# Performance work log

Hardware: AMD Instinct MI355X
Metric: run time of the kernel (lower is better)

Reference implementation:

```python
import jax, jax.numpy as jnp
import numpy as np

CHUNK = 64
L2_EPS = 1e-6
RMS_EPS = 1e-5


def _silu(x):
    return x * jax.nn.sigmoid(x)


def _causal_shared_conv(x, w):
    # x: [B,T,C]; w: [K] single kernel shared across all channels (depthwise).
    K = w.shape[0]
    T = x.shape[1]
    xp = jnp.pad(x, ((0, 0), (K - 1, 0), (0, 0)))
    out = w[0] * xp[:, 0:T, :]
    for j in range(1, K):  # K=4, tiny fixed loop
        out = out + w[j] * xp[:, j:j + T, :]
    return out


def _l2norm(x):
    return x * jax.lax.rsqrt(jnp.sum(x * x, axis=-1, keepdims=True) + L2_EPS)


def _delta_rule_chunk(q, k, v, beta, chunk=CHUNK):
    # q,k: [B,H,T,dk]; v: [B,H,T,dv]; beta: [B,H,T]
    B, H, T, dk = q.shape
    dv = v.shape[-1]
    q = q * (dk ** -0.5)
    nC = T // chunk
    q = q.reshape(B, H, nC, chunk, dk)
    k = k.reshape(B, H, nC, chunk, dk)
    v = v.reshape(B, H, nC, chunk, dv)
    beta = beta.reshape(B, H, nC, chunk)
    k_beta = k * beta[..., None]
    v_beta = v * beta[..., None]
    # UT transform: invert the unit-lower-triangular (I + stril(K_beta K^T))
    A = jnp.einsum('bhncd,bhnmd->bhncm', k_beta, k)  # [B,H,nC,C,C]
    stril = jnp.tril(jnp.ones((chunk, chunk), bool), -1)
    M = jnp.where(stril, A, 0.0) + jnp.eye(chunk, dtype=q.dtype)
    u = jax.scipy.linalg.solve_triangular(M, v_beta, lower=True)  # T @ (beta*v)
    w = jax.scipy.linalg.solve_triangular(M, k_beta, lower=True)  # T @ (beta*k)
    tril_incl = jnp.tril(jnp.ones((chunk, chunk), bool))

    def step(S, inp):
        q_i, k_i, u_i, w_i = inp  # [B,H,C,d*]
        u_i = u_i - jnp.einsum('bhcd,bhde->bhce', w_i, S)
        attn = jnp.where(tril_incl, jnp.einsum('bhcd,bhmd->bhcm', q_i, k_i), 0.0)
        o_i = jnp.einsum('bhcd,bhde->bhce', q_i, S) + jnp.einsum('bhcm,bhme->bhce', attn, u_i)
        S = S + jnp.einsum('bhcd,bhce->bhde', k_i, u_i)
        return S, o_i

    xs = tuple(jnp.moveaxis(t, 2, 0) for t in (q, k, u, w))
    S0 = jnp.zeros((B, H, dk, dv), q.dtype)
    _, o = jax.lax.scan(step, S0, xs)  # o: [nC,B,H,C,dv]
    return jnp.moveaxis(o, 0, 2).reshape(B, H, T, dv)


def setup_inputs() -> dict:
    key = jax.random.key(0)
    ks = jax.random.split(key, 10)
    B, T, D, H = 2, 4096, 2048, 16
    sc = 0.02
    return {
        'x': jax.random.normal(ks[0], (B, T, D), jnp.float32),
        'Wq': jax.random.normal(ks[1], (D, D), jnp.float32) * sc,
        'Wk': jax.random.normal(ks[2], (D, D), jnp.float32) * sc,
        'Wv': jax.random.normal(ks[3], (D, D), jnp.float32) * sc,
        'Wb': jax.random.normal(ks[4], (D, H), jnp.float32) * sc,
        'Wo': jax.random.normal(ks[5], (D, D), jnp.float32) * sc,
        'conv_q': jax.random.normal(ks[6], (4,), jnp.float32) * 0.5,
        'conv_k': jax.random.normal(ks[7], (4,), jnp.float32) * 0.5,
        'conv_v': jax.random.normal(ks[8], (4,), jnp.float32) * 0.5,
        'onorm_w': jnp.ones((D // H,), jnp.float32),
    }


def reference(x, Wq, Wk, Wv, Wb, Wo, conv_q, conv_k, conv_v, onorm_w):
    B, T, D = x.shape
    H = Wb.shape[1]
    dk = Wq.shape[1] // H
    dv = Wv.shape[1] // H
    # projections + shared-kernel causal short conv (silu activation)
    q = _silu(_causal_shared_conv(x @ Wq, conv_q))
    k = _silu(_causal_shared_conv(x @ Wk, conv_k))
    v = _silu(_causal_shared_conv(x @ Wv, conv_v))
    beta = jax.nn.sigmoid(x @ Wb)  # [B,T,H]
    # split heads -> [B,H,T,d]
    qh = _l2norm(q.reshape(B, T, H, dk)).transpose(0, 2, 1, 3)
    kh = _l2norm(k.reshape(B, T, H, dk)).transpose(0, 2, 1, 3)
    vh = v.reshape(B, T, H, dv).transpose(0, 2, 1, 3)
    o = _delta_rule_chunk(qh, kh, vh, beta.transpose(0, 2, 1))  # [B,H,T,dv]
    o = o.transpose(0, 2, 1, 3)  # [B,T,H,dv]
    # per-head RMSNorm over head_v_dim
    o = o * jax.lax.rsqrt(jnp.mean(o * o, axis=-1, keepdims=True) + RMS_EPS) * onorm_w
    return o.reshape(B, T, H * dv) @ Wo
```

## Files before the change

### kernel.cpp

```cpp
#include <hip/hip_runtime.h>
#include <math.h>

#define B_ 2
#define T_ 4096
#define D_ 2048
#define H_ 16
#define DK 128
#define DV 128
#define CH 64
#define M_ (B_ * T_)
#define NCH (T_ / CH)

typedef __attribute__((ext_vector_type(8))) short bfrag;
typedef __attribute__((ext_vector_type(4))) float ffrag;
typedef __attribute__((ext_vector_type(8))) unsigned short u16x8;
typedef unsigned short us;

#define MFMA __builtin_amdgcn_mfma_f32_16x16x32_bf16

__device__ inline us f2bf(float f) {
  union { float f; unsigned u; } v; v.f = f;
  unsigned r = v.u + 0x7fffu + ((v.u >> 16) & 1u);
  return (us)(r >> 16);
}
__device__ inline float bf2f(us u) {
  union { unsigned u; float f; } v; v.u = ((unsigned)u) << 16;
  return v.f;
}

__device__ inline void gl_lds16(const us* g, us* l) {
  __builtin_amdgcn_global_load_lds(
      (const __attribute__((address_space(1))) void*)g,
      (__attribute__((address_space(3))) void*)l, 16, 0, 0);
}

__global__ __launch_bounds__(256) void to_bf16(const float* __restrict__ in,
                                               us* __restrict__ out) {
  const size_t i = ((size_t)blockIdx.x * 256 + threadIdx.x) * 8;
  const float4 a = *reinterpret_cast<const float4*>(in + i);
  const float4 b = *reinterpret_cast<const float4*>(in + i + 4);
  ushort4 o0, o1;
  o0.x = f2bf(a.x); o0.y = f2bf(a.y); o0.z = f2bf(a.z); o0.w = f2bf(a.w);
  o1.x = f2bf(b.x); o1.y = f2bf(b.y); o1.z = f2bf(b.z); o1.w = f2bf(b.w);
  *reinterpret_cast<ushort4*>(out + i) = o0;
  *reinterpret_cast<ushort4*>(out + i + 4) = o1;
}

__global__ __launch_bounds__(256) void wtrans(const float* __restrict__ W,
                                              us* __restrict__ Wt) {
  __shared__ float tile[64][68];
  const int k0 = blockIdx.y * 64, n0 = blockIdx.x * 64;
  const int lr = threadIdx.x >> 4, lc = (threadIdx.x & 15) * 4;
#pragma unroll
  for (int p = 0; p < 4; ++p) {
    const int r = lr + p * 16;
    *reinterpret_cast<float4*>(&tile[r][lc]) =
        *reinterpret_cast<const float4*>(&W[(size_t)(k0 + r) * D_ + n0 + lc]);
  }
  __syncthreads();
#pragma unroll
  for (int p = 0; p < 4; ++p) {
    const int r = lr + p * 16;
    ushort4 o;
    o.x = f2bf(tile[lc + 0][r]); o.y = f2bf(tile[lc + 1][r]);
    o.z = f2bf(tile[lc + 2][r]); o.w = f2bf(tile[lc + 3][r]);
    *reinterpret_cast<ushort4*>(&Wt[(size_t)(n0 + r) * D_ + k0 + lc]) = o;
  }
}

template <bool OUTF32>
__global__ __launch_bounds__(512, 2) void gemm256(const us* __restrict__ A,
                                                  const us* __restrict__ Bt,
                                                  void* __restrict__ Cp,
                                                  int M, int N, int K) {
  __shared__ __align__(16) us lds[2][2][2][256 * 32];
  const int t = threadIdx.x, l = t & 63, w = t >> 6;
  const int wm = w >> 2, wn = w & 3;
  const int fr = l & 15, hi = l >> 4;
  const int sx = 8 * (hi ^ ((fr >> 1) & 3));

  const int m0 = blockIdx.y * 256;
  const int n0 = blockIdx.x * 256;

  const int srow = t >> 2;
  const int scol = 8 * ((t & 3) ^ ((t >> 3) & 3));
  const us* Ab = A + (size_t)(m0 + srow) * K + scol;
  const us* Bb = Bt + (size_t)(n0 + srow) * K + scol;

  ffrag acc[8][4];
#pragma unroll
  for (int mi = 0; mi < 8; ++mi)
#pragma unroll
    for (int ni = 0; ni < 4; ++ni)
#pragma unroll
      for (int e = 0; e < 4; ++e) acc[mi][ni][e] = 0.f;

#define STG_A(bf, kk, kt)                                                      \
  do {                                                                         \
    gl_lds16(Ab + (size_t)(kt) * 64 + (kk) * 32, &lds[bf][0][kk][t * 8]);      \
    gl_lds16(Ab + (size_t)128 * K + (size_t)(kt) * 64 + (kk) * 32,             \
             &lds[bf][0][kk][4096 + t * 8]);                                   \
  } while (0)
#define STG_B(bf, kk, kt)                                                      \
  do {                                                                         \
    gl_lds16(Bb + (size_t)(kt) * 64 + (kk) * 32, &lds[bf][1][kk][t * 8]);      \
    gl_lds16(Bb + (size_t)128 * K + (size_t)(kt) * 64 + (kk) * 32,             \
             &lds[bf][1][kk][4096 + t * 8]);                                   \
  } while (0)

  const int NT = K >> 6;
  STG_A(0, 0, 0); STG_B(0, 0, 0); STG_A(0, 1, 0); STG_B(0, 1, 0);
  asm volatile("s_waitcnt vmcnt(4)" ::: "memory");
  __builtin_amdgcn_s_barrier();
  __builtin_amdgcn_sched_barrier(0);

  const int arow = wm * 128 + fr;
  const int brow = wn * 64 + fr;

#pragma unroll 1
  for (int kt = 0; kt < NT; ++kt) {
    const int cur = kt & 1, oth = cur ^ 1;
    const bool pf = (kt + 1 < NT);
    bfrag af4[4], bf4[4];

    {
      const us* pa = &lds[cur][0][0][0];
      const us* pb = &lds[cur][1][0][0];
#pragma unroll
      for (int ni = 0; ni < 4; ++ni)
        bf4[ni] = *reinterpret_cast<const bfrag*>(pb + (brow + ni * 16) * 32 + sx);
#pragma unroll
      for (int mi = 0; mi < 4; ++mi)
        af4[mi] = *reinterpret_cast<const bfrag*>(pa + (arow + mi * 16) * 32 + sx);
      if (pf) STG_A(oth, 0, kt + 1);
      __builtin_amdgcn_s_setprio(1);
#pragma unroll
      for (int mi = 0; mi < 4; ++mi)
#pragma unroll
        for (int ni = 0; ni < 4; ++ni)
          acc[mi][ni] = MFMA(af4[mi], bf4[ni], acc[mi][ni], 0, 0, 0);
      __builtin_amdgcn_s_setprio(0);
#pragma unroll
      for (int mi = 0; mi < 4; ++mi)
        af4[mi] = *reinterpret_cast<const bfrag*>(pa + (arow + 64 + mi * 16) * 32 + sx);
      if (pf) STG_B(oth, 0, kt + 1);
      __builtin_amdgcn_s_setprio(1);
#pragma unroll
      for (int mi = 0; mi < 4; ++mi)
#pragma unroll
        for (int ni = 0; ni < 4; ++ni)
          acc[mi + 4][ni] = MFMA(af4[mi], bf4[ni], acc[mi + 4][ni], 0, 0, 0);
      __builtin_amdgcn_s_setprio(0);
    }
    if (pf) asm volatile("s_waitcnt vmcnt(4)" ::: "memory");
    else    asm volatile("s_waitcnt vmcnt(0)" ::: "memory");
    __builtin_amdgcn_s_barrier();
    __builtin_amdgcn_sched_barrier(0);

    {
      const us* pa = &lds[cur][0][1][0];
      const us* pb = &lds[cur][1][1][0];
#pragma unroll
      for (int ni = 0; ni < 4; ++ni)
        bf4[ni] = *reinterpret_cast<const bfrag*>(pb + (brow + ni * 16) * 32 + sx);
#pragma unroll
      for (int mi = 0; mi < 4; ++mi)
        af4[mi] = *reinterpret_cast<const bfrag*>(pa + (arow + mi * 16) * 32 + sx);
      if (pf) STG_A(oth, 1, kt + 1);
      __builtin_amdgcn_s_setprio(1);
#pragma unroll
      for (int mi = 0; mi < 4; ++mi)
#pragma unroll
        for (int ni = 0; ni < 4; ++ni)
          acc[mi][ni] = MFMA(af4[mi], bf4[ni], acc[mi][ni], 0, 0, 0);
      __builtin_amdgcn_s_setprio(0);
#pragma unroll
      for (int mi = 0; mi < 4; ++mi)
        af4[mi] = *reinterpret_cast<const bfrag*>(pa + (arow + 64 + mi * 16) * 32 + sx);
      if (pf) STG_B(oth, 1, kt + 1);
      __builtin_amdgcn_s_setprio(1);
#pragma unroll
      for (int mi = 0; mi < 4; ++mi)
#pragma unroll
        for (int ni = 0; ni < 4; ++ni)
          acc[mi + 4][ni] = MFMA(af4[mi], bf4[ni], acc[mi + 4][ni], 0, 0, 0);
      __builtin_amdgcn_s_setprio(0);
    }
    if (pf) asm volatile("s_waitcnt vmcnt(4)" ::: "memory");
    else    asm volatile("s_waitcnt vmcnt(0)" ::: "memory");
    __builtin_amdgcn_s_barrier();
    __builtin_amdgcn_sched_barrier(0);
  }
#undef STG_A
#undef STG_B

  const int crow = m0 + wm * 128 + hi * 4;
  const int ccol = n0 + wn * 64 + fr;
#pragma unroll
  for (int mi = 0; mi < 8; ++mi)
#pragma unroll
    for (int ni = 0; ni < 4; ++ni)
#pragma unroll
      for (int j = 0; j < 4; ++j) {
        const size_t idx = (size_t)(crow + mi * 16 + j) * N + ccol + ni * 16;
        if constexpr (OUTF32) ((float*)Cp)[idx] = acc[mi][ni][j];
        else ((us*)Cp)[idx] = f2bf(acc[mi][ni][j]);
      }
}

__device__ inline void conv_body(const us* __restrict__ in, const float* cw,
                                 int bt, int d0, int mode, float v[8]) {
  const int tb = bt & (T_ - 1);
  const us* row = in + (size_t)bt * D_ + d0;
#pragma unroll
  for (int j = 0; j < 8; ++j) v[j] = 0.f;
#pragma unroll
  for (int j = 0; j < 4; ++j) {
    if (tb >= j) {
      const us* rp = row - (size_t)(j * D_);
      const ushort4 a = *reinterpret_cast<const ushort4*>(rp);
      const ushort4 b = *reinterpret_cast<const ushort4*>(rp + 4);
      const float wj = cw[3 - j];
      v[0] = fmaf(wj, bf2f(a.x), v[0]); v[1] = fmaf(wj, bf2f(a.y), v[1]);
      v[2] = fmaf(wj, bf2f(a.z), v[2]); v[3] = fmaf(wj, bf2f(a.w), v[3]);
      v[4] = fmaf(wj, bf2f(b.x), v[4]); v[5] = fmaf(wj, bf2f(b.y), v[5]);
      v[6] = fmaf(wj, bf2f(b.z), v[6]); v[7] = fmaf(wj, bf2f(b.w), v[7]);
    }
  }
#pragma unroll
  for (int j = 0; j < 8; ++j) v[j] = v[j] / (1.f + expf(-v[j]));
  if (mode) {
    float ss = 0.f;
#pragma unroll
    for (int j = 0; j < 8; ++j) ss = fmaf(v[j], v[j], ss);
    ss += __shfl_xor(ss, 1);
    ss += __shfl_xor(ss, 2);
    ss += __shfl_xor(ss, 4);
    ss += __shfl_xor(ss, 8);
    float sc = rsqrtf(ss + 1e-6f);
    if (mode == 2) sc *= 0.08838834764831845f;
#pragma unroll
    for (int j = 0; j < 8; ++j) v[j] *= sc;
  }
}

__global__ __launch_bounds__(256) void conv_silu_plain(const us* __restrict__ in,
                                                       const float* __restrict__ cw,
                                                       us* __restrict__ out) {
  const int bt = blockIdx.x, d0 = threadIdx.x * 8;
  float v[8];
  conv_body(in, cw, bt, d0, 0, v);
  ushort4 o0, o1;
  o0.x = f2bf(v[0]); o0.y = f2bf(v[1]); o0.z = f2bf(v[2]); o0.w = f2bf(v[3]);
  o1.x = f2bf(v[4]); o1.y = f2bf(v[5]); o1.z = f2bf(v[6]); o1.w = f2bf(v[7]);
  us* op = out + (size_t)bt * D_ + d0;
  *reinterpret_cast<ushort4*>(op) = o0;
  *reinterpret_cast<ushort4*>(op + 4) = o1;
}

__global__ __launch_bounds__(256) void conv_silu_chunk(const us* __restrict__ in,
                                                       const float* __restrict__ cw,
                                                       us* __restrict__ out,
                                                       int mode) {
  const int bt = blockIdx.x, d0 = threadIdx.x * 8;
  float v[8];
  conv_body(in, cw, bt, d0, mode, v);
  const int b = bt >> 12, tt = bt & (T_ - 1);
  const int cid = tt >> 6, r = tt & 63;
  const int h = d0 >> 7, g = (d0 & 127) >> 3;
  us* dst = out + ((size_t)((b * H_ + h) * NCH + cid)) * (CH * DK) +
            r * 128 + ((g ^ (r & 15)) * 8);
  ushort4 o0, o1;
  o0.x = f2bf(v[0]); o0.y = f2bf(v[1]); o0.z = f2bf(v[2]); o0.w = f2bf(v[3]);
  o1.x = f2bf(v[4]); o1.y = f2bf(v[5]); o1.z = f2bf(v[6]); o1.w = f2bf(v[7]);
  *reinterpret_cast<ushort4*>(dst) = o0;
  *reinterpret_cast<ushort4*>(dst + 4) = o1;
}

__global__ __launch_bounds__(256) void beta_sigmoid(const float* __restrict__ x,
                                                    const float* __restrict__ Wb,
                                                    float* __restrict__ betaT) {
  const int t = threadIdx.x;
  const int m = blockIdx.x * 4 + (t >> 6);
  const int l = t & 63;
  const int c = l & 15;
  const int s = l >> 4;
  const float* xr = x + (size_t)m * D_;
  const int kb = s * (D_ / 4);
  float acc = 0.f;
  for (int k = 0; k < D_ / 4; ++k)
    acc = fmaf(xr[kb + k], Wb[(size_t)(kb + k) * H_ + c], acc);
  acc += __shfl_xor(acc, 16);
  acc += __shfl_xor(acc, 32);
  if (l < 16) {
    const int b = m >> 12, tt = m & (T_ - 1);
    betaT[((size_t)(b * H_ + c)) * T_ + tt] = 1.f / (1.f + expf(-acc));
  }
}

__device__ inline void prod_step(float* Tf, const float* Am, float* xbuf,
                                 int r, int c, int I, int J,
                                 int nk, int K0, int K1, int K2) {
  float X = 0.f;
  const int Ks[3] = {K0, K1, K2};
  for (int kk = 0; kk < nk; ++kk) {
    const int K = Ks[kk];
    const float* amrow = Am + (16 * I + r) * 72 + 16 * K;
    const float* tcol = Tf + (16 * K) * 68 + 16 * J + c;
#pragma unroll
    for (int m = 0; m < 16; ++m) X = fmaf(amrow[m], tcol[m * 68], X);
  }
  __syncthreads();
  xbuf[r * 17 + c] = X;
  __syncthreads();
  float s = 0.f;
  const float* trow = Tf + (16 * I + r) * 68 + 16 * I;
#pragma unroll
  for (int m = 0; m < 16; ++m) s = fmaf(trow[m], xbuf[m * 17 + c], s);
  Tf[(16 * I + r) * 68 + 16 * J + c] = -s;
  __syncthreads();
}

__global__ __launch_bounds__(256, 2) void delta_prep(const us* __restrict__ qch,
                                                     const us* __restrict__ kch,
                                                     const float* __restrict__ betaT,
                                                     us* __restrict__ v_uv,
                                                     us* __restrict__ Wout,
                                                     us* __restrict__ kTout,
                                                     us* __restrict__ Aout) {
  __shared__ __align__(16) unsigned char lds[72000];
  us*    ks    = (us*)(lds);
  us*    Tb    = (us*)(lds);
  float* Am    = (float*)(lds + 16384);
  us*    vTb   = (us*)(lds + 16384);
  float* Tf    = (float*)(lds + 34816);
  us*    atst  = (us*)(lds + 34816);
  us*    Wst   = (us*)(lds + 34816);
  us*    kTb   = (us*)(lds + 52224);
  us*    UVst  = (us*)(lds + 52224);
  float* betac = (float*)(lds + 70656);
  float* xbuf  = (float*)(lds + 70912);

  const int t = threadIdx.x, w = t >> 6, l = t & 63;
  const int rr = l & 15, hi = l >> 4;
  const int bx = blockIdx.x;
  const int bh = bx >> 6, cid = bx & 63;
  const int b = bh >> 4, h = bh & 15;
  const size_t rowbase = ((size_t)b * T_ + (size_t)cid * CH) * D_ + (size_t)h * DK;
  const size_t cbase = (size_t)bx * (CH * DK);
  const size_t abase = (size_t)bx * (CH * CH);

  {
    const us* kg = kch + cbase;
#pragma unroll
    for (int p = 0; p < 4; ++p)
      gl_lds16(kg + p * 2048 + t * 8, ks + p * 2048 + t * 8);
    const float4 z = make_float4(0.f, 0.f, 0.f, 0.f);
    *reinterpret_cast<float4*>(atst + t * 16) = z;
    *reinterpret_cast<float4*>(atst + t * 16 + 8) = z;
    if (t < 64) betac[t] = betaT[(size_t)bh * T_ + cid * CH + t];
  }
  __syncthreads();

  {
    bfrag qf[4], kf[4];
#pragma unroll
    for (int k4 = 0; k4 < 4; ++k4) {
      const int go = ((4 * k4 + hi) ^ rr) * 8;
      qf[k4] = *reinterpret_cast<const bfrag*>(qch + cbase + (16 * w + rr) * 128 + go);
      kf[k4] = *reinterpret_cast<const bfrag*>(ks + (16 * w + rr) * 128 + go);
    }
    for (int jt = 0; jt <= w; ++jt) {
      ffrag accA = {0.f, 0.f, 0.f, 0.f}, accQ = {0.f, 0.f, 0.f, 0.f};
#pragma unroll
      for (int k4 = 0; k4 < 4; ++k4) {
        const bfrag bfr = *reinterpret_cast<const bfrag*>(
            ks + (16 * jt + rr) * 128 + (((4 * k4 + hi) ^ rr) * 8));
        accA = MFMA(kf[k4], bfr, accA, 0, 0, 0);
        accQ = MFMA(qf[k4], bfr, accQ, 0, 0, 0);
      }
// ... 61 lines not shown
    const int vr = t >> 2, vp = t & 3;
    u16x8 vv[4];
#pragma unroll
    for (int g = 0; g < 4; ++g)
      vv[g] = *reinterpret_cast<const u16x8*>(v_uv + rowbase + (size_t)vr * D_ +
                                              vp * 32 + g * 8);
    const int ti = t >> 2, tg = t & 3;
    u16x8 w0, w1;
#pragma unroll
    for (int jj = 0; jj < 8; ++jj) {
      const int j0 = tg * 16 + jj, j1 = j0 + 8;
      w0[jj] = f2bf(Tf[ti * 68 + j0] * betac[j0]);
      w1[jj] = f2bf(Tf[ti * 68 + j1] * betac[j1]);
    }
    *reinterpret_cast<u16x8*>(Tb + ti * 72 + tg * 16) = w0;
    *reinterpret_cast<u16x8*>(Tb + ti * 72 + tg * 16 + 8) = w1;
#pragma unroll
    for (int g = 0; g < 4; ++g)
#pragma unroll
      for (int j = 0; j < 8; ++j)
        vTb[(vp * 32 + g * 8 + j) * 72 + vr] = vv[g][j];
  }
  __syncthreads();

  {
    bfrag ta[2];
#pragma unroll
    for (int k2 = 0; k2 < 2; ++k2)
      ta[k2] = *reinterpret_cast<const bfrag*>(Tb + (16 * w + rr) * 72 + 32 * k2 + 8 * hi);
#pragma unroll
    for (int dt = 0; dt < 8; ++dt) {
      ffrag acc = {0.f, 0.f, 0.f, 0.f};
#pragma unroll
      for (int k2 = 0; k2 < 2; ++k2) {
        const bfrag bfr = *reinterpret_cast<const bfrag*>(
            kTb + (16 * dt + rr) * 72 + 32 * k2 + 8 * hi);
        acc = MFMA(ta[k2], bfr, acc, 0, 0, 0);
      }
#pragma unroll
      for (int j4 = 0; j4 < 4; ++j4) {
        const int i = 16 * w + 4 * hi + j4, d = 16 * dt + rr;
        Wst[i * 128 + (((d >> 3) ^ (i & 15)) * 8) + (d & 7)] = f2bf(-acc[j4]);
      }
    }
  }
  __syncthreads();

  {
    bfrag ta[2];
#pragma unroll
    for (int k2 = 0; k2 < 2; ++k2)
      ta[k2] = *reinterpret_cast<const bfrag*>(Tb + (16 * w + rr) * 72 + 32 * k2 + 8 * hi);
#pragma unroll
    for (int et = 0; et < 8; ++et) {
      ffrag acc = {0.f, 0.f, 0.f, 0.f};
#pragma unroll
      for (int k2 = 0; k2 < 2; ++k2) {
        const bfrag bfr = *reinterpret_cast<const bfrag*>(
            vTb + (16 * et + rr) * 72 + 32 * k2 + 8 * hi);
        acc = MFMA(ta[k2], bfr, acc, 0, 0, 0);
      }
#pragma unroll
      for (int j4 = 0; j4 < 4; ++j4)
        UVst[(16 * w + 4 * hi + j4) * 128 + 16 * et + rr] = f2bf(acc[j4]);
    }
#pragma unroll
    for (int p = 0; p < 4; ++p) {
      const int unit = t + p * 256;
      *reinterpret_cast<u16x8*>(Wout + cbase + unit * 8) =
          *reinterpret_cast<const u16x8*>(Wst + unit * 8);
    }
  }
  __syncthreads();

#pragma unroll
  for (int p = 0; p < 4; ++p) {
    const int unit = t + p * 256;
    const int r = unit >> 4, g = unit & 15;
    *reinterpret_cast<u16x8*>(v_uv + rowbase + (size_t)r * D_ + g * 8) =
        *reinterpret_cast<const u16x8*>(UVst + r * 128 + g * 8);
  }
}

__global__ __launch_bounds__(256, 1) void delta_seq(const us* __restrict__ qch,
                                                    const us* __restrict__ Wch,
                                                    const us* __restrict__ kTch,
                                                    const us* __restrict__ atch,
                                                    us* __restrict__ uv_o) {
  __shared__ __align__(16) us qs[2][CH * DK];
  __shared__ __align__(16) us Ws[2][CH * DK];
  __shared__ __align__(16) us kTs[2][DK * CH];
  __shared__ __align__(16) us ats[2][CH * CH];
  __shared__ __align__(16) us uvs[2][CH * 16];
  __shared__ __align__(16) us Sb[2][16 * 136];
  __shared__ __align__(16) us ub[CH * 18];

  const int t = threadIdx.x, l = t & 63, w = t >> 6;
  const int bx = blockIdx.x;
  const int vs = bx >> 5, bh = bx & 31;
  const int b = bh >> 4, h = bh & 15;
  const int rr = l & 15, hi = l >> 4;

  ffrag sacc[2];
#pragma unroll
  for (int t2 = 0; t2 < 2; ++t2)
#pragma unroll
    for (int j = 0; j < 4; ++j) sacc[t2][j] = 0.f;

  for (int i = t; i < 16 * 136; i += 256) Sb[0][i] = 0;

  const size_t cbQ = (size_t)(bh * NCH) * (CH * DK);
  const size_t cbA = (size_t)(bh * NCH) * (CH * CH);
  const size_t rowbase0 = ((size_t)b * T_) * D_ + (size_t)h * DK + vs * 16;

#define STAGE(buf, cid)                                                        \
  do {                                                                         \
    const us* qg = qch + cbQ + (size_t)(cid) * (CH * DK);                      \
    const us* Wg = Wch + cbQ + (size_t)(cid) * (CH * DK);                      \
    const us* kg = kTch + cbQ + (size_t)(cid) * (CH * DK);                     \
    const us* ag = atch + cbA + (size_t)(cid) * (CH * CH);                     \
    _Pragma("unroll")                                                          \
    for (int p = 0; p < 4; ++p) {                                              \
      gl_lds16(qg + p * 2048 + t * 8, &qs[buf][p * 2048 + t * 8]);             \
      gl_lds16(Wg + p * 2048 + t * 8, &Ws[buf][p * 2048 + t * 8]);             \
      gl_lds16(kg + p * 2048 + t * 8, &kTs[buf][p * 2048 + t * 8]);            \
    }                                                                          \
    _Pragma("unroll")                                                          \
    for (int p = 0; p < 2; ++p)                                                \
      gl_lds16(ag + p * 2048 + t * 8, &ats[buf][p * 2048 + t * 8]);            \
    if (t < 128)                                                               \
      gl_lds16(uv_o + rowbase0 + (size_t)((cid) * CH + (t >> 1)) * D_ + (t & 1) * 8, \
               &uvs[buf][t * 8]);                                              \
  } while (0)

  STAGE(0, 0);
  asm volatile("s_waitcnt vmcnt(0) lgkmcnt(0)" ::: "memory");
  __builtin_amdgcn_s_barrier();
  __builtin_amdgcn_sched_barrier(0);

  for (int cid = 0; cid < NCH; ++cid) {
    const int cur = cid & 1;
    if (cid + 1 < NCH) STAGE(cur ^ 1, cid + 1);

    bfrag sbf[4];
#pragma unroll
    for (int ks = 0; ks < 4; ++ks)
      sbf[ks] = *reinterpret_cast<const bfrag*>(&Sb[cur][rr * 136 + ks * 32 + hi * 8]);

    {
      ffrag uacc;
#pragma unroll
      for (int j = 0; j < 4; ++j)
        uacc[j] = bf2f(uvs[cur][(16 * w + 4 * hi + j) * 16 + rr]);
#pragma unroll
      for (int ks = 0; ks < 4; ++ks) {
        const bfrag af = *reinterpret_cast<const bfrag*>(
            &Ws[cur][(16 * w + rr) * 128 + (((4 * ks + hi) ^ rr) * 8)]);
        uacc = MFMA(af, sbf[ks], uacc, 0, 0, 0);
      }
#pragma unroll
      for (int j = 0; j < 4; ++j)
        ub[(16 * w + 4 * hi + j) * 18 + rr] = f2bf(uacc[j]);
    }
    asm volatile("s_waitcnt lgkmcnt(0)" ::: "memory");
    __builtin_amdgcn_s_barrier();
    __builtin_amdgcn_sched_barrier(0);

    {
      ffrag oacc;
#pragma unroll
      for (int j = 0; j < 4; ++j) oacc[j] = 0.f;
#pragma unroll
      for (int ks = 0; ks < 4; ++ks) {
        const bfrag af = *reinterpret_cast<const bfrag*>(
            &qs[cur][(16 * w + rr) * 128 + (((4 * ks + hi) ^ rr) * 8)]);
        oacc = MFMA(af, sbf[ks], oacc, 0, 0, 0);
      }
      const int nks = (w < 2) ? 1 : 2;
      for (int ks = 0; ks < nks; ++ks) {
        bfrag ubf;
#pragma unroll
        for (int j = 0; j < 8; ++j)
          ubf[j] = (short)ub[(32 * ks + 8 * hi + j) * 18 + rr];
        const bfrag af = *reinterpret_cast<const bfrag*>(
            &ats[cur][(16 * w + rr) * 64 + (((4 * ks + hi) ^ (rr & 7)) * 8)]);
        oacc = MFMA(af, ubf, oacc, 0, 0, 0);
      }
      us* og = uv_o + rowbase0 + (size_t)(cid * CH) * D_;
#pragma unroll
      for (int j = 0; j < 4; ++j)
        og[(size_t)(16 * w + 4 * hi + j) * D_ + rr] = f2bf(oacc[j]);
    }

    {
      bfrag ubf[2];
#pragma unroll
      for (int ks = 0; ks < 2; ++ks)
#pragma unroll
        for (int j = 0; j < 8; ++j)
          ubf[ks][j] = (short)ub[(32 * ks + 8 * hi + j) * 18 + rr];
#pragma unroll
      for (int t2 = 0; t2 < 2; ++t2) {
        const int tile = 2 * w + t2;
#pragma unroll
        for (int ks = 0; ks < 2; ++ks) {
          const bfrag af = *reinterpret_cast<const bfrag*>(
              &kTs[cur][(16 * tile + rr) * 64 + (((4 * ks + hi) ^ (rr & 7)) * 8)]);
          sacc[t2] = MFMA(af, ubf[ks], sacc[t2], 0, 0, 0);
        }
        ushort4 sw;
        sw.x = f2bf(sacc[t2][0]); sw.y = f2bf(sacc[t2][1]);
        sw.z = f2bf(sacc[t2][2]); sw.w = f2bf(sacc[t2][3]);
        *reinterpret_cast<ushort4*>(&Sb[cur ^ 1][rr * 136 + 16 * tile + 4 * hi]) = sw;
      }
    }
    asm volatile("s_waitcnt vmcnt(0) lgkmcnt(0)" ::: "memory");
    __builtin_amdgcn_s_barrier();
    __builtin_amdgcn_sched_barrier(0);
  }
#undef STAGE
}

__global__ __launch_bounds__(256) void rms_onorm_bf16(const us* __restrict__ in,
                                                      const float* __restrict__ w,
                                                      us* __restrict__ out) {
  const int bt = blockIdx.x;
  const int d0 = threadIdx.x * 8;
  const us* p = in + (size_t)bt * D_ + d0;
  const ushort4 a = *reinterpret_cast<const ushort4*>(p);
  const ushort4 b = *reinterpret_cast<const ushort4*>(p + 4);
  float v[8] = {bf2f(a.x), bf2f(a.y), bf2f(a.z), bf2f(a.w),
                bf2f(b.x), bf2f(b.y), bf2f(b.z), bf2f(b.w)};
  float ss = 0.f;
#pragma unroll
  for (int j = 0; j < 8; ++j) ss = fmaf(v[j], v[j], ss);
  ss += __shfl_xor(ss, 1);
  ss += __shfl_xor(ss, 2);
  ss += __shfl_xor(ss, 4);
  ss += __shfl_xor(ss, 8);
  const float sc = rsqrtf(ss * (1.0f / 128.0f) + 1e-5f);
  const int hd = d0 & 127;
  ushort4 o0, o1;
  o0.x = f2bf(v[0] * sc * w[hd + 0]); o0.y = f2bf(v[1] * sc * w[hd + 1]);
  o0.z = f2bf(v[2] * sc * w[hd + 2]); o0.w = f2bf(v[3] * sc * w[hd + 3]);
  o1.x = f2bf(v[4] * sc * w[hd + 4]); o1.y = f2bf(v[5] * sc * w[hd + 5]);
  o1.z = f2bf(v[6] * sc * w[hd + 6]); o1.w = f2bf(v[7] * sc * w[hd + 7]);
  us* op = out + (size_t)bt * D_ + d0;
  *reinterpret_cast<ushort4*>(op) = o0;
  *reinterpret_cast<ushort4*>(op + 4) = o1;
}

extern "C" void kernel_launch(void* const* d_in, const int* in_sizes, int n_in,
                              void* d_out, int out_size, void* d_ws, size_t ws_size,
                              hipStream_t stream) {
  const float* x  = (const float*)d_in[0];
  const float* Wq = (const float*)d_in[1];
  const float* Wk = (const float*)d_in[2];
  const float* Wv = (const float*)d_in[3];
  const float* Wb = (const float*)d_in[4];
  const float* Wo = (const float*)d_in[5];
  const float* cq = (const float*)d_in[6];
  const float* ck = (const float*)d_in[7];
  const float* cv = (const float*)d_in[8];
  const float* ow = (const float*)d_in[9];
  float* out = (float*)d_out;

  const size_t NE = (size_t)M_ * D_;
  us* ws   = (us*)d_ws;
  us* gout = ws;
  us* qch  = ws + NE;
  us* kch  = ws + 2 * NE;
  us* Wch  = ws + 3 * NE;
  us* kTch = ws + 4 * NE;
  us* wt   = ws + 5 * NE;
  us* attb = gout;
  float* betaT = (float*)(gout + 12 * 1024 * 1024);
  us* xb = (us*)d_out;
  us* vb = xb + NE;

  dim3 gg(D_ / 256, M_ / 256);
  dim3 wg(D_ / 64, D_ / 64);

  to_bf16<<<NE / 2048, 256, 0, stream>>>(x, xb);

  wtrans<<<wg, 256, 0, stream>>>(Wv, wt);
  gemm256<false><<<gg, 512, 0, stream>>>(xb, wt, gout, M_, D_, D_);
  conv_silu_plain<<<M_, 256, 0, stream>>>(gout, cv, vb);

  wtrans<<<wg, 256, 0, stream>>>(Wq, wt);
  gemm256<false><<<gg, 512, 0, stream>>>(xb, wt, gout, M_, D_, D_);
  conv_silu_chunk<<<M_, 256, 0, stream>>>(gout, cq, qch, 2);

  wtrans<<<wg, 256, 0, stream>>>(Wk, wt);
  gemm256<false><<<gg, 512, 0, stream>>>(xb, wt, gout, M_, D_, D_);
  conv_silu_chunk<<<M_, 256, 0, stream>>>(gout, ck, kch, 1);

  beta_sigmoid<<<M_ / 4, 256, 0, stream>>>(x, Wb, betaT);

  delta_prep<<<32 * NCH, 256, 0, stream>>>(qch, kch, betaT, vb, Wch, kTch, attb);
  delta_seq<<<256, 256, 0, stream>>>(qch, Wch, kTch, attb, vb);

  rms_onorm_bf16<<<M_, 256, 0, stream>>>(vb, ow, kTch);

  wtrans<<<wg, 256, 0, stream>>>(Wo, wt);
  gemm256<true><<<gg, 512, 0, stream>>>(kTch, wt, out, M_, D_, D_);
}
```

Baseline: 650.9 us.

## Split delta_seq into 512-thread specialized warps for state update and output

The sequential delta-rule kernel now launches 512 threads. Warps 0-3 compute u and the state update, while warps 4-7 compute the chunk output (q·S plus attn·u) in parallel instead of serially in the same warps. Output tiles are staged in LDS and written to global memory one iteration later with vectorized stores. The betaT buffer moves to a separate workspace region, and the kernel-definition order is reshuffled. This raises the thread count and adds LDS use, and the extra waves add barrier cost on a latency-bound serial loop.

```diff
diff --git a/kernel.cpp b/kernel.cpp
--- a/kernel.cpp
+++ b/kernel.cpp
@@ -44,237 +44,6 @@
   o1.x = f2bf(b.x); o1.y = f2bf(b.y); o1.z = f2bf(b.z); o1.w = f2bf(b.w);
   *reinterpret_cast<ushort4*>(out + i) = o0;
   *reinterpret_cast<ushort4*>(out + i + 4) = o1;
-}
-
-__global__ __launch_bounds__(256) void wtrans(const float* __restrict__ W,
-                                              us* __restrict__ Wt) {
-  __shared__ float tile[64][68];
-  const int k0 = blockIdx.y * 64, n0 = blockIdx.x * 64;
-  const int lr = threadIdx.x >> 4, lc = (threadIdx.x & 15) * 4;
-#pragma unroll
-  for (int p = 0; p < 4; ++p) {
-    const int r = lr + p * 16;
-    *reinterpret_cast<float4*>(&tile[r][lc]) =
-        *reinterpret_cast<const float4*>(&W[(size_t)(k0 + r) * D_ + n0 + lc]);
-  }
-  __syncthreads();
-#pragma unroll
-  for (int p = 0; p < 4; ++p) {
-    const int r = lr + p * 16;
-    ushort4 o;
-    o.x = f2bf(tile[lc + 0][r]); o.y = f2bf(tile[lc + 1][r]);
-    o.z = f2bf(tile[lc + 2][r]); o.w = f2bf(tile[lc + 3][r]);
-    *reinterpret_cast<ushort4*>(&Wt[(size_t)(n0 + r) * D_ + k0 + lc]) = o;
-  }
-}
-
-template <bool OUTF32>
-__global__ __launch_bounds__(512, 2) void gemm256(const us* __restrict__ A,
-                                                  const us* __restrict__ Bt,
-                                                  void* __restrict__ Cp,
-                                                  int M, int N, int K) {
-  __shared__ __align__(16) us lds[2][2][2][256 * 32];
-  const int t = threadIdx.x, l = t & 63, w = t >> 6;
-  const int wm = w >> 2, wn = w & 3;
-  const int fr = l & 15, hi = l >> 4;
-  const int sx = 8 * (hi ^ ((fr >> 1) & 3));
-
-  const int m0 = blockIdx.y * 256;
-  const int n0 = blockIdx.x * 256;
-
-  const int srow = t >> 2;
-  const int scol = 8 * ((t & 3) ^ ((t >> 3) & 3));
-  const us* Ab = A + (size_t)(m0 + srow) * K + scol;
-  const us* Bb = Bt + (size_t)(n0 + srow) * K + scol;
-
-  ffrag acc[8][4];
-#pragma unroll
-  for (int mi = 0; mi < 8; ++mi)
-#pragma unroll
-    for (int ni = 0; ni < 4; ++ni)
-#pragma unroll
-      for (int e = 0; e < 4; ++e) acc[mi][ni][e] = 0.f;
-
-#define STG_A(bf, kk, kt)                                                      \
-  do {                                                                         \
-    gl_lds16(Ab + (size_t)(kt) * 64 + (kk) * 32, &lds[bf][0][kk][t * 8]);      \
-    gl_lds16(Ab + (size_t)128 * K + (size_t)(kt) * 64 + (kk) * 32,             \
-             &lds[bf][0][kk][4096 + t * 8]);                                   \
-  } while (0)
-#define STG_B(bf, kk, kt)                                                      \
-  do {                                                                         \
-    gl_lds16(Bb + (size_t)(kt) * 64 + (kk) * 32, &lds[bf][1][kk][t * 8]);      \
-    gl_lds16(Bb + (size_t)128 * K + (size_t)(kt) * 64 + (kk) * 32,             \
-             &lds[bf][1][kk][4096 + t * 8]);                                   \
-  } while (0)
-
-  const int NT = K >> 6;
-  STG_A(0, 0, 0); STG_B(0, 0, 0); STG_A(0, 1, 0); STG_B(0, 1, 0);
-  asm volatile("s_waitcnt vmcnt(4)" ::: "memory");
-  __builtin_amdgcn_s_barrier();
-  __builtin_amdgcn_sched_barrier(0);
-
-  const int arow = wm * 128 + fr;
-  const int brow = wn * 64 + fr;
-
-#pragma unroll 1
-  for (int kt = 0; kt < NT; ++kt) {
-    const int cur = kt & 1, oth = cur ^ 1;
-    const bool pf = (kt + 1 < NT);
-    bfrag af4[4], bf4[4];
-
-    {
-      const us* pa = &lds[cur][0][0][0];
-      const us* pb = &lds[cur][1][0][0];
-#pragma unroll
-      for (int ni = 0; ni < 4; ++ni)
-        bf4[ni] = *reinterpret_cast<const bfrag*>(pb + (brow + ni * 16) * 32 + sx);
-#pragma unroll
-      for (int mi = 0; mi < 4; ++mi)
-        af4[mi] = *reinterpret_cast<const bfrag*>(pa + (arow + mi * 16) * 32 + sx);
-      if (pf) STG_A(oth, 0, kt + 1);
-      __builtin_amdgcn_s_setprio(1);
-#pragma unroll
-      for (int mi = 0; mi < 4; ++mi)
-#pragma unroll
-        for (int ni = 0; ni < 4; ++ni)
-          acc[mi][ni] = MFMA(af4[mi], bf4[ni], acc[mi][ni], 0, 0, 0);
-      __builtin_amdgcn_s_setprio(0);
-#pragma unroll
-      for (int mi = 0; mi < 4; ++mi)
-        af4[mi] = *reinterpret_cast<const bfrag*>(pa + (arow + 64 + mi * 16) * 32 + sx);
-      if (pf) STG_B(oth, 0, kt + 1);
-      __builtin_amdgcn_s_setprio(1);
-#pragma unroll
-      for (int mi = 0; mi < 4; ++mi)
-#pragma unroll
-        for (int ni = 0; ni < 4; ++ni)
-          acc[mi + 4][ni] = MFMA(af4[mi], bf4[ni], acc[mi + 4][ni], 0, 0, 0);
-      __builtin_amdgcn_s_setprio(0);
-    }
-    if (pf) asm volatile("s_waitcnt vmcnt(4)" ::: "memory");
-    else    asm volatile("s_waitcnt vmcnt(0)" ::: "memory");
-    __builtin_amdgcn_s_barrier();
-    __builtin_amdgcn_sched_barrier(0);
-
-    {
-      const us* pa = &lds[cur][0][1][0];
-      const us* pb = &lds[cur][1][1][0];
-#pragma unroll
-      for (int ni = 0; ni < 4; ++ni)
-        bf4[ni] = *reinterpret_cast<const bfrag*>(pb + (brow + ni * 16) * 32 + sx);
-#pragma unroll
-      for (int mi = 0; mi < 4; ++mi)
-        af4[mi] = *reinterpret_cast<const bfrag*>(pa + (arow + mi * 16) * 32 + sx);
-      if (pf) STG_A(oth, 1, kt + 1);
-      __builtin_amdgcn_s_setprio(1);
-#pragma unroll
-      for (int mi = 0; mi < 4; ++mi)
-#pragma unroll
-        for (int ni = 0; ni < 4; ++ni)
-          acc[mi][ni] = MFMA(af4[mi], bf4[ni], acc[mi][ni], 0, 0, 0);
-      __builtin_amdgcn_s_setprio(0);
-#pragma unroll
-      for (int mi = 0; mi < 4; ++mi)
-        af4[mi] = *reinterpret_cast<const bfrag*>(pa + (arow + 64 + mi * 16) * 32 + sx);
-      if (pf) STG_B(oth, 1, kt + 1);
-      __builtin_amdgcn_s_setprio(1);
-#pragma unroll
-      for (int mi = 0; mi < 4; ++mi)
-#pragma unroll
-        for (int ni = 0; ni < 4; ++ni)
-          acc[mi + 4][ni] = MFMA(af4[mi], bf4[ni], acc[mi + 4][ni], 0, 0, 0);
-      __builtin_amdgcn_s_setprio(0);
-    }
-    if (pf) asm volatile("s_waitcnt vmcnt(4)" ::: "memory");
-    else    asm volatile("s_waitcnt vmcnt(0)" ::: "memory");
-    __builtin_amdgcn_s_barrier();
-    __builtin_amdgcn_sched_barrier(0);
-  }
-#undef STG_A
-#undef STG_B
-
-  const int crow = m0 + wm * 128 + hi * 4;
-  const int ccol = n0 + wn * 64 + fr;
-#pragma unroll
-  for (int mi = 0; mi < 8; ++mi)
-#pragma unroll
-    for (int ni = 0; ni < 4; ++ni)
-#pragma unroll
-      for (int j = 0; j < 4; ++j) {
-        const size_t idx = (size_t)(crow + mi * 16 + j) * N + ccol + ni * 16;
-        if constexpr (OUTF32) ((float*)Cp)[idx] = acc[mi][ni][j];
-        else ((us*)Cp)[idx] = f2bf(acc[mi][ni][j]);
-      }
-}
-
-__device__ inline void conv_body(const us* __restrict__ in, const float* cw,
-                                 int bt, int d0, int mode, float v[8]) {
-  const int tb = bt & (T_ - 1);
-  const us* row = in + (size_t)bt * D_ + d0;
-#pragma unroll
-  for (int j = 0; j < 8; ++j) v[j] = 0.f;
-#pragma unroll
-  for (int j = 0; j < 4; ++j) {
-    if (tb >= j) {
-      const us* rp = row - (size_t)(j * D_);
-      const ushort4 a = *reinterpret_cast<const ushort4*>(rp);
-      const ushort4 b = *reinterpret_cast<const ushort4*>(rp + 4);
-      const float wj = cw[3 - j];
-      v[0] = fmaf(wj, bf2f(a.x), v[0]); v[1] = fmaf(wj, bf2f(a.y), v[1]);
-      v[2] = fmaf(wj, bf2f(a.z), v[2]); v[3] = fmaf(wj, bf2f(a.w), v[3]);
-      v[4] = fmaf(wj, bf2f(b.x), v[4]); v[5] = fmaf(wj, bf2f(b.y), v[5]);
-      v[6] = fmaf(wj, bf2f(b.z), v[6]); v[7] = fmaf(wj, bf2f(b.w), v[7]);
-    }
-  }
-#pragma unroll
-  for (int j = 0; j < 8; ++j) v[j] = v[j] / (1.f + expf(-v[j]));
-  if (mode) {
-    float ss = 0.f;
-#pragma unroll
-    for (int j = 0; j < 8; ++j) ss = fmaf(v[j], v[j], ss);
-    ss += __shfl_xor(ss, 1);
-    ss += __shfl_xor(ss, 2);
-    ss += __shfl_xor(ss, 4);
-    ss += __shfl_xor(ss, 8);
-    float sc = rsqrtf(ss + 1e-6f);
-    if (mode == 2) sc *= 0.08838834764831845f;
-#pragma unroll
-    for (int j = 0; j < 8; ++j) v[j] *= sc;
-  }
-}
-
-__global__ __launch_bounds__(256) void conv_silu_plain(const us* __restrict__ in,
-                                                       const float* __restrict__ cw,
-                                                       us* __restrict__ out) {
-  const int bt = blockIdx.x, d0 = threadIdx.x * 8;
-  float v[8];
-  conv_body(in, cw, bt, d0, 0, v);
-  ushort4 o0, o1;
-  o0.x = f2bf(v[0]); o0.y = f2bf(v[1]); o0.z = f2bf(v[2]); o0.w = f2bf(v[3]);
-  o1.x = f2bf(v[4]); o1.y = f2bf(v[5]); o1.z = f2bf(v[6]); o1.w = f2bf(v[7]);
-  us* op = out + (size_t)bt * D_ + d0;
-  *reinterpret_cast<ushort4*>(op) = o0;
-  *reinterpret_cast<ushort4*>(op + 4) = o1;
-}
-
-__global__ __launch_bounds__(256) void conv_silu_chunk(const us* __restrict__ in,
-                                                       const float* __restrict__ cw,
-                                                       us* __restrict__ out,
-                                                       int mode) {
-  const int bt = blockIdx.x, d0 = threadIdx.x * 8;
-  float v[8];
-  conv_body(in, cw, bt, d0, mode, v);
-  const int b = bt >> 12, tt = bt & (T_ - 1);
-  const int cid = tt >> 6, r = tt & 63;
-  const int h = d0 >> 7, g = (d0 & 127) >> 3;
-  us* dst = out + ((size_t)((b * H_ + h) * NCH + cid)) * (CH * DK) +
-            r * 128 + ((g ^ (r & 15)) * 8);
-  ushort4 o0, o1;
-  o0.x = f2bf(v[0]); o0.y = f2bf(v[1]); o0.z = f2bf(v[2]); o0.w = f2bf(v[3]);
-  o1.x = f2bf(v[4]); o1.y = f2bf(v[5]); o1.z = f2bf(v[6]); o1.w = f2bf(v[7]);
-  *reinterpret_cast<ushort4*>(dst) = o0;
-  *reinterpret_cast<ushort4*>(dst + 4) = o1;
 }
 
 __global__ __launch_bounds__(256) void beta_sigmoid(const float* __restrict__ x,
@@ -296,6 +65,237 @@
     const int b = m >> 12, tt = m & (T_ - 1);
     betaT[((size_t)(b * H_ + c)) * T_ + tt] = 1.f / (1.f + expf(-acc));
   }
+}
+
+__global__ __launch_bounds__(256) void wtrans(const float* __restrict__ W,
+                                              us* __restrict__ Wt) {
+  __shared__ float tile[64][68];
+  const int k0 = blockIdx.y * 64, n0 = blockIdx.x * 64;
+  const int lr = threadIdx.x >> 4, lc = (threadIdx.x & 15) * 4;
+#pragma unroll
+  for (int p = 0; p < 4; ++p) {
+    const int r = lr + p * 16;
+    *reinterpret_cast<float4*>(&tile[r][lc]) =
+        *reinterpret_cast<const float4*>(&W[(size_t)(k0 + r) * D_ + n0 + lc]);
+  }
+  __syncthreads();
+#pragma unroll
+  for (int p = 0; p < 4; ++p) {
+    const int r = lr + p * 16;
+    ushort4 o;
+    o.x = f2bf(tile[lc + 0][r]); o.y = f2bf(tile[lc + 1][r]);
+    o.z = f2bf(tile[lc + 2][r]); o.w = f2bf(tile[lc + 3][r]);
+    *reinterpret_cast<ushort4*>(&Wt[(size_t)(n0 + r) * D_ + k0 + lc]) = o;
+  }
+}
+
+template <bool OUTF32>
+__global__ __launch_bounds__(512, 2) void gemm256(const us* __restrict__ A,
+                                                  const us* __restrict__ Bt,
+                                                  void* __restrict__ Cp,
+                                                  int M, int N, int K) {
+  __shared__ __align__(16) us lds[2][2][2][256 * 32];
+  const int t = threadIdx.x, l = t & 63, w = t >> 6;
+  const int wm = w >> 2, wn = w & 3;
+  const int fr = l & 15, hi = l >> 4;
+  const int sx = 8 * (hi ^ ((fr >> 1) & 3));
+
+  const int m0 = blockIdx.y * 256;
+  const int n0 = blockIdx.x * 256;
+
+  const int srow = t >> 2;
+  const int scol = 8 * ((t & 3) ^ ((t >> 3) & 3));
+  const us* Ab = A + (size_t)(m0 + srow) * K + scol;
+  const us* Bb = Bt + (size_t)(n0 + srow) * K + scol;
+
+  ffrag acc[8][4];
+#pragma unroll
+  for (int mi = 0; mi < 8; ++mi)
+#pragma unroll
+    for (int ni = 0; ni < 4; ++ni)
+#pragma unroll
+      for (int e = 0; e < 4; ++e) acc[mi][ni][e] = 0.f;
+
+#define STG_A(bf, kk, kt)                                                      \
+  do {                                                                         \
+    gl_lds16(Ab + (size_t)(kt) * 64 + (kk) * 32, &lds[bf][0][kk][t * 8]);      \
+    gl_lds16(Ab + (size_t)128 * K + (size_t)(kt) * 64 + (kk) * 32,             \
+             &lds[bf][0][kk][4096 + t * 8]);                                   \
+  } while (0)
+#define STG_B(bf, kk, kt)                                                      \
+  do {                                                                         \
+    gl_lds16(Bb + (size_t)(kt) * 64 + (kk) * 32, &lds[bf][1][kk][t * 8]);      \
+    gl_lds16(Bb + (size_t)128 * K + (size_t)(kt) * 64 + (kk) * 32,             \
+             &lds[bf][1][kk][4096 + t * 8]);                                   \
+  } while (0)
+
+  const int NT = K >> 6;
+  STG_A(0, 0, 0); STG_B(0, 0, 0); STG_A(0, 1, 0); STG_B(0, 1, 0);
+  asm volatile("s_waitcnt vmcnt(4)" ::: "memory");
+  __builtin_amdgcn_s_barrier();
+  __builtin_amdgcn_sched_barrier(0);
+
+  const int arow = wm * 128 + fr;
+  const int brow = wn * 64 + fr;
+
+#pragma unroll 1
+  for (int kt = 0; kt < NT; ++kt) {
+    const int cur = kt & 1, oth = cur ^ 1;
+    const bool pf = (kt + 1 < NT);
+    bfrag af4[4], bf4[4];
+
+    {
+      const us* pa = &lds[cur][0][0][0];
+      const us* pb = &lds[cur][1][0][0];
+#pragma unroll
+      for (int ni = 0; ni < 4; ++ni)
+        bf4[ni] = *reinterpret_cast<const bfrag*>(pb + (brow + ni * 16) * 32 + sx);
+#pragma unroll
+      for (int mi = 0; mi < 4; ++mi)
+        af4[mi] = *reinterpret_cast<const bfrag*>(pa + (arow + mi * 16) * 32 + sx);
+      if (pf) STG_A(oth, 0, kt + 1);
+      __builtin_amdgcn_s_setprio(1);
+#pragma unroll
+      for (int mi = 0; mi < 4; ++mi)
+#pragma unroll
+        for (int ni = 0; ni < 4; ++ni)
+          acc[mi][ni] = MFMA(af4[mi], bf4[ni], acc[mi][ni], 0, 0, 0);
+      __builtin_amdgcn_s_setprio(0);
+#pragma unroll
+      for (int mi = 0; mi < 4; ++mi)
+        af4[mi] = *reinterpret_cast<const bfrag*>(pa + (arow + 64 + mi * 16) * 32 + sx);
+      if (pf) STG_B(oth, 0, kt + 1);
+      __builtin_amdgcn_s_setprio(1);
+#pragma unroll
+      for (int mi = 0; mi < 4; ++mi)
+#pragma unroll
+        for (int ni = 0; ni < 4; ++ni)
+          acc[mi + 4][ni] = MFMA(af4[mi], bf4[ni], acc[mi + 4][ni], 0, 0, 0);
+      __builtin_amdgcn_s_setprio(0);
+    }
+    if (pf) asm volatile("s_waitcnt vmcnt(4)" ::: "memory");
+    else    asm volatile("s_waitcnt vmcnt(0)" ::: "memory");
+    __builtin_amdgcn_s_barrier();
+    __builtin_amdgcn_sched_barrier(0);
+
+    {
+      const us* pa = &lds[cur][0][1][0];
+      const us* pb = &lds[cur][1][1][0];
+#pragma unroll
+      for (int ni = 0; ni < 4; ++ni)
+        bf4[ni] = *reinterpret_cast<const bfrag*>(pb + (brow + ni * 16) * 32 + sx);
+#pragma unroll
+      for (int mi = 0; mi < 4; ++mi)
+        af4[mi] = *reinterpret_cast<const bfrag*>(pa + (arow + mi * 16) * 32 + sx);
+      if (pf) STG_A(oth, 1, kt + 1);
+      __builtin_amdgcn_s_setprio(1);
+#pragma unroll
+      for (int mi = 0; mi < 4; ++mi)
+#pragma unroll
+        for (int ni = 0; ni < 4; ++ni)
+          acc[mi][ni] = MFMA(af4[mi], bf4[ni], acc[mi][ni], 0, 0, 0);
+      __builtin_amdgcn_s_setprio(0);
+#pragma unroll
+      for (int mi = 0; mi < 4; ++mi)
+        af4[mi] = *reinterpret_cast<const bfrag*>(pa + (arow + 64 + mi * 16) * 32 + sx);
+      if (pf) STG_B(oth, 1, kt + 1);
+      __builtin_amdgcn_s_setprio(1);
+#pragma unroll
+      for (int mi = 0; mi < 4; ++mi)
+#pragma unroll
+        for (int ni = 0; ni < 4; ++ni)
+          acc[mi + 4][ni] = MFMA(af4[mi], bf4[ni], acc[mi + 4][ni], 0, 0, 0);
+      __builtin_amdgcn_s_setprio(0);
+    }
+    if (pf) asm volatile("s_waitcnt vmcnt(4)" ::: "memory");
+    else    asm volatile("s_waitcnt vmcnt(0)" ::: "memory");
+    __builtin_amdgcn_s_barrier();
+    __builtin_amdgcn_sched_barrier(0);
+  }
+#undef STG_A
+#undef STG_B
+
+  const int crow = m0 + wm * 128 + hi * 4;
+  const int ccol = n0 + wn * 64 + fr;
+#pragma unroll
+  for (int mi = 0; mi < 8; ++mi)
+#pragma unroll
+    for (int ni = 0; ni < 4; ++ni)
+#pragma unroll
+      for (int j = 0; j < 4; ++j) {
+        const size_t idx = (size_t)(crow + mi * 16 + j) * N + ccol + ni * 16;
+        if constexpr (OUTF32) ((float*)Cp)[idx] = acc[mi][ni][j];
+        else ((us*)Cp)[idx] = f2bf(acc[mi][ni][j]);
+      }
+}
+
+__device__ inline void conv_body(const us* __restrict__ in, const float* cw,
+                                 int bt, int d0, int mode, float v[8]) {
+  const int tb = bt & (T_ - 1);
+  const us* row = in + (size_t)bt * D_ + d0;
+#pragma unroll
+  for (int j = 0; j < 8; ++j) v[j] = 0.f;
+#pragma unroll
+  for (int j = 0; j < 4; ++j) {
+    if (tb >= j) {
+      const us* rp = row - (size_t)(j * D_);
+      const ushort4 a = *reinterpret_cast<const ushort4*>(rp);
+      const ushort4 b = *reinterpret_cast<const ushort4*>(rp + 4);
+      const float wj = cw[3 - j];
+      v[0] = fmaf(wj, bf2f(a.x), v[0]); v[1] = fmaf(wj, bf2f(a.y), v[1]);
+      v[2] = fmaf(wj, bf2f(a.z), v[2]); v[3] = fmaf(wj, bf2f(a.w), v[3]);
+      v[4] = fmaf(wj, bf2f(b.x), v[4]); v[5] = fmaf(wj, bf2f(b.y), v[5]);
+      v[6] = fmaf(wj, bf2f(b.z), v[6]); v[7] = fmaf(wj, bf2f(b.w), v[7]);
+    }
+  }
+#pragma unroll
+  for (int j = 0; j < 8; ++j) v[j] = v[j] / (1.f + expf(-v[j]));
+  if (mode) {
+    float ss = 0.f;
+#pragma unroll
+    for (int j = 0; j < 8; ++j) ss = fmaf(v[j], v[j], ss);
+    ss += __shfl_xor(ss, 1);
+    ss += __shfl_xor(ss, 2);
+    ss += __shfl_xor(ss, 4);
+    ss += __shfl_xor(ss, 8);
+    float sc = rsqrtf(ss + 1e-6f);
+    if (mode == 2) sc *= 0.08838834764831845f;
+#pragma unroll
+    for (int j = 0; j < 8; ++j) v[j] *= sc;
+  }
+}
+
+__global__ __launch_bounds__(256) void conv_silu_plain(const us* __restrict__ in,
+                                                       const float* __restrict__ cw,
+                                                       us* __restrict__ out) {
+  const int bt = blockIdx.x, d0 = threadIdx.x * 8;
+  float v[8];
+  conv_body(in, cw, bt, d0, 0, v);
+  ushort4 o0, o1;
+  o0.x = f2bf(v[0]); o0.y = f2bf(v[1]); o0.z = f2bf(v[2]); o0.w = f2bf(v[3]);
+  o1.x = f2bf(v[4]); o1.y = f2bf(v[5]); o1.z = f2bf(v[6]); o1.w = f2bf(v[7]);
+  us* op = out + (size_t)bt * D_ + d0;
+  *reinterpret_cast<ushort4*>(op) = o0;
+  *reinterpret_cast<ushort4*>(op + 4) = o1;
+}
+
+__global__ __launch_bounds__(256) void conv_silu_chunk(const us* __restrict__ in,
+                                                       const float* __restrict__ cw,
+                                                       us* __restrict__ out,
+                                                       int mode) {
+  const int bt = blockIdx.x, d0 = threadIdx.x * 8;
+  float v[8];
+  conv_body(in, cw, bt, d0, mode, v);
+  const int b = bt >> 12, tt = bt & (T_ - 1);
+  const int cid = tt >> 6, r = tt & 63;
+  const int h = d0 >> 7, g = (d0 & 127) >> 3;
+  us* dst = out + ((size_t)((b * H_ + h) * NCH + cid)) * (CH * DK) +
+            r * 128 + ((g ^ (r & 15)) * 8);
+  ushort4 o0, o1;
+  o0.x = f2bf(v[0]); o0.y = f2bf(v[1]); o0.z = f2bf(v[2]); o0.w = f2bf(v[3]);
+  o1.x = f2bf(v[4]); o1.y = f2bf(v[5]); o1.z = f2bf(v[6]); o1.w = f2bf(v[7]);
+  *reinterpret_cast<ushort4*>(dst) = o0;
+  *reinterpret_cast<ushort4*>(dst + 4) = o1;
 }
 
 __device__ inline void prod_step(float* Tf, const float* Am, float* xbuf,
@@ -523,7 +523,7 @@
   }
 }
 
-__global__ __launch_bounds__(256, 1) void delta_seq(const us* __restrict__ qch,
+__global__ __launch_bounds__(512, 1) void delta_seq(const us* __restrict__ qch,
                                                     const us* __restrict__ Wch,
                                                     const us* __restrict__ kTch,
                                                     const us* __restrict__ atch,
@@ -535,12 +535,14 @@
   __shared__ __align__(16) us uvs[2][CH * 16];
   __shared__ __align__(16) us Sb[2][16 * 136];
   __shared__ __align__(16) us ub[CH * 18];
+  __shared__ __align__(16) us ob[CH * 18];
 
   const int t = threadIdx.x, l = t & 63, w = t >> 6;
   const int bx = blockIdx.x;
   const int vs = bx >> 5, bh = bx & 31;
   const int b = bh >> 4, h = bh & 15;
   const int rr = l & 15, hi = l >> 4;
+  const int w2 = w & 3;
 
   ffrag sacc[2];
 #pragma unroll
@@ -548,7 +550,7 @@
 #pragma unroll
     for (int j = 0; j < 4; ++j) sacc[t2][j] = 0.f;
 
-  for (int i = t; i < 16 * 136; i += 256) Sb[0][i] = 0;
+  for (int i = t; i < 16 * 136; i += 512) Sb[0][i] = 0;
 
   const size_t cbQ = (size_t)(bh * NCH) * (CH * DK);
   const size_t cbA = (size_t)(bh * NCH) * (CH * CH);
@@ -560,15 +562,13 @@
     const us* Wg = Wch + cbQ + (size_t)(cid) * (CH * DK);                      \
     const us* kg = kTch + cbQ + (size_t)(cid) * (CH * DK);                     \
     const us* ag = atch + cbA + (size_t)(cid) * (CH * CH);                     \
-    _Pragma("unroll")                                                          \
-    for (int p = 0; p < 4; ++p) {                                              \
-      gl_lds16(qg + p * 2048 + t * 8, &qs[buf][p * 2048 + t * 8]);             \
-      gl_lds16(Wg + p * 2048 + t * 8, &Ws[buf][p * 2048 + t * 8]);             \
-      gl_lds16(kg + p * 2048 + t * 8, &kTs[buf][p * 2048 + t * 8]);            \
-    }                                                                          \
-    _Pragma("unroll")                                                          \
-    for (int p = 0; p < 2; ++p)                                                \
-      gl_lds16(ag + p * 2048 + t * 8, &ats[buf][p * 2048 + t * 8]);            \
+    gl_lds16(qg + t * 8, &qs[buf][t * 8]);                                     \
+    gl_lds16(qg + 4096 + t * 8, &qs[buf][4096 + t * 8]);                       \
+    gl_lds16(Wg + t * 8, &Ws[buf][t * 8]);                                     \
+    gl_lds16(Wg + 4096 + t * 8, &Ws[buf][4096 + t * 8]);                       \
+    gl_lds16(kg + t * 8, &kTs[buf][t * 8]);                                    \
+    gl_lds16(kg + 4096 + t * 8, &kTs[buf][4096 + t * 8]);                      \
+    gl_lds16(ag + t * 8, &ats[buf][t * 8]);                                    \
     if (t < 128)                                                               \
       gl_lds16(uv_o + rowbase0 + (size_t)((cid) * CH + (t >> 1)) * D_ + (t & 1) * 8, \
                &uvs[buf][t * 8]);                                              \
@@ -581,6 +581,12 @@
 
   for (int cid = 0; cid < NCH; ++cid) {
     const int cur = cid & 1;
+
+    if (cid > 0 && t < 128) {
+      const u16x8 ov = *reinterpret_cast<const u16x8*>(&ob[(t >> 1) * 18 + (t & 1) * 8]);
+      *reinterpret_cast<u16x8*>(uv_o + rowbase0 +
+          (size_t)((cid - 1) * CH + (t >> 1)) * D_ + (t & 1) * 8) = ov;
+    }
     if (cid + 1 < NCH) STAGE(cur ^ 1, cid + 1);
 
     bfrag sbf[4];
@@ -588,52 +594,35 @@
     for (int ks = 0; ks < 4; ++ks)
       sbf[ks] = *reinterpret_cast<const bfrag*>(&Sb[cur][rr * 136 + ks * 32 + hi * 8]);
 
-    {
-      ffrag uacc;
+    ffrag acc4;
+    if (w < 4) {
 #pragma unroll
       for (int j = 0; j < 4; ++j)
-        uacc[j] = bf2f(uvs[cur][(16 * w + 4 * hi + j) * 16 + rr]);
+        acc4[j] = bf2f(uvs[cur][(16 * w + 4 * hi + j) * 16 + rr]);
 #pragma unroll
       for (int ks = 0; ks < 4; ++ks) {
         const bfrag af = *reinterpret_cast<const bfrag*>(
             &Ws[cur][(16 * w + rr) * 128 + (((4 * ks + hi) ^ rr) * 8)]);
-        uacc = MFMA(af, sbf[ks], uacc, 0, 0, 0);
+        acc4 = MFMA(af, sbf[ks], acc4, 0, 0, 0);
       }
 #pragma unroll
       for (int j = 0; j < 4; ++j)
-        ub[(16 * w + 4 * hi + j) * 18 + rr] = f2bf(uacc[j]);
+        ub[(16 * w + 4 * hi + j) * 18 + rr] = f2bf(acc4[j]);
+    } else {
+#pragma unroll
+      for (int j = 0; j < 4; ++j) acc4[j] = 0.f;
+#pragma unroll
+      for (int ks = 0; ks < 4; ++ks) {
+        const bfrag af = *reinterpret_cast<const bfrag*>(
+            &qs[cur][(16 * w2 + rr) * 128 + (((4 * ks + hi) ^ rr) * 8)]);
+        acc4 = MFMA(af, sbf[ks], acc4, 0, 0, 0);
+      }
     }
     asm volatile("s_waitcnt lgkmcnt(0)" ::: "memory");
     __builtin_amdgcn_s_barrier();
     __builtin_amdgcn_sched_barrier(0);
 
-    {
-      ffrag oacc;
-#pragma unroll
-      for (int j = 0; j < 4; ++j) oacc[j] = 0.f;
-#pragma unroll
-      for (int ks = 0; ks < 4; ++ks) {
-        const bfrag af = *reinterpret_cast<const bfrag*>(
-            &qs[cur][(16 * w + rr) * 128 + (((4 * ks + hi) ^ rr) * 8)]);
-        oacc = MFMA(af, sbf[ks], oacc, 0, 0, 0);
-      }
-      const int nks = (w < 2) ? 1 : 2;
-      for (int ks = 0; ks < nks; ++ks) {
-        bfrag ubf;
-#pragma unroll
-        for (int j = 0; j < 8; ++j)
-          ubf[j] = (short)ub[(32 * ks + 8 * hi + j) * 18 + rr];
-        const bfrag af = *reinterpret_cast<const bfrag*>(
-            &ats[cur][(16 * w + rr) * 64 + (((4 * ks + hi) ^ (rr & 7)) * 8)]);
-        oacc = MFMA(af, ubf, oacc, 0, 0, 0);
-      }
-      us* og = uv_o + rowbase0 + (size_t)(cid * CH) * D_;
-#pragma unroll
-      for (int j = 0; j < 4; ++j)
-        og[(size_t)(16 * w + 4 * hi + j) * D_ + rr] = f2bf(oacc[j]);
-    }
-
-    {
+    if (w < 4) {
       bfrag ubf[2];
 #pragma unroll
       for (int ks = 0; ks < 2; ++ks)
@@ -654,12 +643,32 @@
         sw.z = f2bf(sacc[t2][2]); sw.w = f2bf(sacc[t2][3]);
         *reinterpret_cast<ushort4*>(&Sb[cur ^ 1][rr * 136 + 16 * tile + 4 * hi]) = sw;
       }
+    } else {
+      const int nks = (w2 < 2) ? 1 : 2;
+      for (int ks = 0; ks < nks; ++ks) {
+        bfrag ubf;
+#pragma unroll
+        for (int j = 0; j < 8; ++j)
+          ubf[j] = (short)ub[(32 * ks + 8 * hi + j) * 18 + rr];
+        const bfrag af = *reinterpret_cast<const bfrag*>(
+            &ats[cur][(16 * w2 + rr) * 64 + (((4 * ks + hi) ^ (rr & 7)) * 8)]);
+        acc4 = MFMA(af, ubf, acc4, 0, 0, 0);
+      }
+#pragma unroll
+      for (int j = 0; j < 4; ++j)
+        ob[(16 * w2 + 4 * hi + j) * 18 + rr] = f2bf(acc4[j]);
     }
     asm volatile("s_waitcnt vmcnt(0) lgkmcnt(0)" ::: "memory");
     __builtin_amdgcn_s_barrier();
     __builtin_amdgcn_sched_barrier(0);
   }
 #undef STAGE
+
+  if (t < 128) {
+    const u16x8 ov = *reinterpret_cast<const u16x8*>(&ob[(t >> 1) * 18 + (t & 1) * 8]);
+    *reinterpret_cast<u16x8*>(uv_o + rowbase0 +
+        (size_t)((NCH - 1) * CH + (t >> 1)) * D_ + (t & 1) * 8) = ov;
+  }
 }
 
 __global__ __launch_bounds__(256) void rms_onorm_bf16(const us* __restrict__ in,
@@ -715,7 +724,7 @@
   us* kTch = ws + 4 * NE;
   us* wt   = ws + 5 * NE;
   us* attb = gout;
-  float* betaT = (float*)(gout + 12 * 1024 * 1024);
+  float* betaT = (float*)(ws + 5 * NE + (size_t)D_ * D_);
   us* xb = (us*)d_out;
   us* vb = xb + NE;
 
@@ -739,7 +748,7 @@
   beta_sigmoid<<<M_ / 4, 256, 0, stream>>>(x, Wb, betaT);
 
   delta_prep<<<32 * NCH, 256, 0, stream>>>(qch, kch, betaT, vb, Wch, kTch, attb);
-  delta_seq<<<256, 256, 0, stream>>>(qch, Wch, kTch, attb, vb);
+  delta_seq<<<256, 512, 0, stream>>>(qch, Wch, kTch, attb, vb);
 
   rms_onorm_bf16<<<M_, 256, 0, stream>>>(vb, ow, kTch);
 
```

New measurement: 636.6 us. 2.2% less time.
